# Kernel tuning notes

Hardware: AMD Instinct MI355X
Metric: run time of the kernel (lower is better)

The kernel has to match this reference:

```python
import jax, jax.numpy as jnp
import numpy as np

# dims: T frames, node counts per type, edge counts per relation
T, NA, ND, NB = 48, 1024, 1024, 128
IN, H, HT, OUT = 16, 128, 256, 128
E_AA, E_AD, E_DD, E_AB, E_DB = 8192, 8192, 8192, 2048, 2048


def setup_inputs() -> dict:
    key = jax.random.key(0)
    ks = iter(jax.random.split(key, 48))

    def nrm(shape, scale=0.05):
        return jax.random.normal(next(ks), shape, jnp.float32) * scale

    def edges(e, ns, nd):
        src = jax.random.randint(next(ks), (e,), 0, ns)
        dst = jax.random.randint(next(ks), (e,), 0, nd)
        return jnp.stack([src, dst]).astype(jnp.int32)

    return dict(
        x_attk=jax.random.normal(next(ks), (T, NA, IN), jnp.float32),
        x_def=jax.random.normal(next(ks), (T, ND, IN), jnp.float32),
        x_ball=jax.random.normal(next(ks), (T, NB, IN), jnp.float32),
        ei_aa=edges(E_AA, NA, NA),
        ei_ad=edges(E_AD, NA, ND),
        ei_dd=edges(E_DD, ND, ND),
        ei_ab=edges(E_AB, NA, NB),
        ei_db=edges(E_DB, ND, NB),
        Wp_a=nrm((IN, H)), bp_a=nrm((H,)),
        Wp_d=nrm((IN, H)), bp_d=nrm((H,)),
        Wp_b=nrm((IN, H)), bp_b=nrm((H,)),
        Wg_aa=nrm((H, H)), bg_aa=nrm((H,)),
        Wg_dd=nrm((H, H)), bg_dd=nrm((H,)),
        Wl_ad=nrm((H, H)), Wr_ad=nrm((H, H)), bl_ad=nrm((H,)),
        Wl_ab=nrm((H, H)), Wr_ab=nrm((H, H)), bl_ab=nrm((H,)),
        Wl_db=nrm((H, H)), Wr_db=nrm((H, H)), bl_db=nrm((H,)),
        Wi=nrm((H, 3 * HT)), Wh=nrm((HT, 3 * HT)),
        bi=nrm((3 * HT,)), bh=nrm((3 * HT,)),
        Wout=nrm((3 * HT, OUT)), bout=nrm((OUT,)),
    )


def gcn(x, ei, W, b, n):
    # PyG GCNConv, add_self_loops=False: x' = D^-1/2 A D^-1/2 (x W) + b
    row, col = ei[0], ei[1]
    deg = jnp.zeros((n,), x.dtype).at[col].add(1.0)
    dis = jnp.where(deg > 0, 1.0 / jnp.sqrt(jnp.maximum(deg, 1.0)), 0.0)
    norm = dis[row] * dis[col]                      # [E]
    xw = x @ W                                       # [T, n, H]
    msg = xw[:, row] * norm[None, :, None]           # [T, E, H]
    return jnp.zeros_like(xw).at[:, col].add(msg) + b


def sage(x_src, x_dst, ei, Wl, bl, Wr, nd):
    # PyG SAGEConv (mean aggr): out = mean_j x_j Wl + bl + x_i Wr
    row, col = ei[0], ei[1]
    cnt = jnp.zeros((nd,), x_src.dtype).at[col].add(1.0)
    s = jnp.zeros((x_src.shape[0], nd, x_src.shape[-1]), x_src.dtype)
    s = s.at[:, col].add(x_src[:, row])
    mean = s / jnp.maximum(cnt, 1.0)[None, :, None]
    return mean @ Wl + bl + x_dst @ Wr


def gru_last(z_seq, Wi, Wh, bi, bh):
    # torch GRU (1 layer) final hidden state; z_seq: [T, N, H]
    ht = Wh.shape[0]

    def step(h, x):
        gi = x @ Wi + bi
        gh = h @ Wh + bh
        ir, iz, inn = jnp.split(gi, 3, axis=-1)
        hr, hz, hn = jnp.split(gh, 3, axis=-1)
        r = jax.nn.sigmoid(ir + hr)
        z = jax.nn.sigmoid(iz + hz)
        ncand = jnp.tanh(inn + r * hn)
        return (1.0 - z) * ncand + z * h, None

    h0 = jnp.zeros((z_seq.shape[1], ht), z_seq.dtype)
    hT, _ = jax.lax.scan(step, h0, z_seq)
    return hT                                        # [N, HT]


def _forward(x_attk, x_def, x_ball, ei_aa, ei_ad, ei_dd, ei_ab, ei_db,
             Wp_a, bp_a, Wp_d, bp_d, Wp_b, bp_b,
             Wg_aa, bg_aa, Wg_dd, bg_dd,
             Wl_ad, Wr_ad, bl_ad, Wl_ab, Wr_ab, bl_ab, Wl_db, Wr_db, bl_db,
             Wi, Wh, bi, bh, Wout, bout):
    # per-type node projection (all frames at once)
    pa = x_attk @ Wp_a + bp_a                        # [T, NA, H]
    pd = x_def @ Wp_d + bp_d
    pb = x_ball @ Wp_b + bp_b
    # HeteroConv with sum aggregation across relations per dst type
    z_a = gcn(pa, ei_aa, Wg_aa, bg_aa, NA)
    z_d = gcn(pd, ei_dd, Wg_dd, bg_dd, ND) + sage(pa, pd, ei_ad, Wl_ad, bl_ad, Wr_ad, ND)
    z_b = sage(pa, pb, ei_ab, Wl_ab, bl_ab, Wr_ab, NB) + sage(pd, pb, ei_db, Wl_db, bl_db, Wr_db, NB)
    # temporal GRU over frames, pool final hidden over nodes
    pooled = [gru_last(z, Wi, Wh, bi, bh).mean(axis=0) for z in (z_a, z_d, z_b)]
    return jnp.concatenate(pooled, axis=-1) @ Wout + bout   # [OUT]


def reference(x_attk, x_def, x_ball, ei_aa, ei_ad, ei_dd, ei_ab, ei_db,
              Wp_a, bp_a, Wp_d, bp_d, Wp_b, bp_b,
              Wg_aa, bg_aa, Wg_dd, bg_dd,
              Wl_ad, Wr_ad, bl_ad, Wl_ab, Wr_ab, bl_ab, Wl_db, Wr_db, bl_db,
              Wi, Wh, bi, bh, Wout, bout):
    return _forward(x_attk, x_def, x_ball, ei_aa, ei_ad, ei_dd, ei_ab, ei_db,
                    Wp_a, bp_a, Wp_d, bp_d, Wp_b, bp_b,
                    Wg_aa, bg_aa, Wg_dd, bg_dd,
                    Wl_ad, Wr_ad, bl_ad, Wl_ab, Wr_ab, bl_ab, Wl_db, Wr_db, bl_db,
                    Wi, Wh, bi, bh, Wout, bout)
```

## Files before the change

kernel.cpp:

```cpp
#include <hip/hip_runtime.h>
#include <math.h>

#define TT   48
#define NAA  1024
#define NDD  1024
#define NBB  128
#define NTT  2176
#define INF  16
#define HH   128
#define HTT  256
#define GG   768
#define OUTF 128
#define EAA  8192
#define EAD  8192
#define EDD  8192
#define EAB  2048
#define EDB  2048
#define NEDGE (EAA + EDD + EAD + EAB + EDB)
#define NGRP 136
#define TCH  8

typedef short bf16x8 __attribute__((ext_vector_type(8)));
typedef float f32x4  __attribute__((ext_vector_type(4)));

static const size_t SZ_PB   = (size_t)TT * NTT * HH;
static const size_t OFF_PB  = 0;
static const size_t OFF_ZB  = OFF_PB + SZ_PB / 2;
static const size_t OFF_H0  = OFF_ZB + SZ_PB / 2;
static const size_t OFF_BA  = OFF_H0 + (size_t)NTT * HTT / 2;
static const size_t OFF_BB  = OFF_BA + GG;
static const size_t OFF_WTG = OFF_BB + GG;
static const size_t OFF_BT  = OFF_WTG + 57344;
static const size_t OFF_WIP = OFF_BT + 384;
static const size_t OFF_WHP = OFF_WIP + 49152;
static const size_t OFF_POOL= OFF_WHP + 98304;
static const size_t OFF_PART= OFF_POOL + 1024;
static const size_t OFF_STATS = OFF_PART + 34816;
static const size_t SZ_GI1  = (size_t)TCH * NGRP * 48 * 256 / 2;
static const size_t OFF_GI0 = OFF_STATS + 58400;
static const size_t OFF_GI1 = OFF_GI0 + SZ_GI1;

enum {
  S_CNT_AA=0, S_CNT_DD=1024, S_CNT_AD=2048, S_CNT_AB=3072, S_CNT_DB=3200,
  S_CUR_AA=3328, S_CUR_DD=4352, S_CUR_AD=5376, S_CUR_AB=6400, S_CUR_DB=6528,
  S_ZERO_END=6656,
  S_OFF_AA=6656, S_OFF_DD=7684, S_OFF_AD=8712, S_OFF_AB=9740, S_OFF_DB=9872,
  S_SRC_AA=10004, S_SRC_DD=18196, S_SRC_AD=26388, S_SRC_AB=34580, S_SRC_DB=36628,
  S_NRM_AA=38676, S_NRM_DD=46868,
  S_DIS_AA=55060, S_DIS_DD=56084, S_INV_AD=57108, S_INV_AB=58132, S_INV_DB=58260,
  S_END=58388
};

__device__ __forceinline__ unsigned short f2b(float x) {
  union { float f; unsigned int u; } v; v.f = x;
  unsigned int r = v.u + 0x7FFFu + ((v.u >> 16) & 1u);
  return (unsigned short)(r >> 16);
}
__device__ __forceinline__ float b2f(unsigned short b) {
  union { unsigned int u; float f; } v; v.u = ((unsigned int)b) << 16;
  return v.f;
}

__global__ void count_all(const int* __restrict__ aa, const int* __restrict__ dd,
                          const int* __restrict__ ad, const int* __restrict__ ab,
                          const int* __restrict__ db, int* __restrict__ st) {
  int e = blockIdx.x * 256 + threadIdx.x;
  if (e < EAA) atomicAdd(&st[S_CNT_AA + aa[EAA + e]], 1);
  else if (e < EAA + EDD) atomicAdd(&st[S_CNT_DD + dd[EDD + (e - EAA)]], 1);
  else if (e < EAA + EDD + EAD) atomicAdd(&st[S_CNT_AD + ad[EAD + (e - EAA - EDD)]], 1);
  else if (e < EAA + EDD + EAD + EAB) atomicAdd(&st[S_CNT_AB + ab[EAB + (e - EAA - EDD - EAD)]], 1);
  else if (e < NEDGE) atomicAdd(&st[S_CNT_DB + db[EDB + (e - EAA - EDD - EAD - EAB)]], 1);
}

__global__ __launch_bounds__(1024) void scan5(int* __restrict__ st) {
  __shared__ int buf[1024];
  int b = blockIdx.x, i = threadIdx.x;
  int n, coff, ooff, uoff, soff, isGcn;
  switch (b) {
    case 0:  n = 1024; coff = S_CNT_AA; ooff = S_OFF_AA; uoff = S_CUR_AA; soff = S_DIS_AA; isGcn = 1; break;
    case 1:  n = 1024; coff = S_CNT_DD; ooff = S_OFF_DD; uoff = S_CUR_DD; soff = S_DIS_DD; isGcn = 1; break;
    case 2:  n = 1024; coff = S_CNT_AD; ooff = S_OFF_AD; uoff = S_CUR_AD; soff = S_INV_AD; isGcn = 0; break;
    case 3:  n = 128;  coff = S_CNT_AB; ooff = S_OFF_AB; uoff = S_CUR_AB; soff = S_INV_AB; isGcn = 0; break;
    default: n = 128;  coff = S_CNT_DB; ooff = S_OFF_DB; uoff = S_CUR_DB; soff = S_INV_DB; isGcn = 0; break;
  }
  float* stf = (float*)st;
  int c = (i < n) ? st[coff + i] : 0;
  buf[i] = c;
  __syncthreads();
  for (int s = 1; s < 1024; s <<= 1) {
    int tv = (i >= s) ? buf[i - s] : 0;
    __syncthreads();
    buf[i] += tv;
    __syncthreads();
  }
  if (i < n) {
    int excl = buf[i] - c;
    st[ooff + i] = excl;
    st[uoff + i] = excl;
    if (i == n - 1) st[ooff + n] = buf[i];
    if (isGcn) stf[soff + i] = (c > 0) ? (1.0f / sqrtf((float)c)) : 0.0f;
    else       stf[soff + i] = 1.0f / (float)(c > 0 ? c : 1);
  }
}

__global__ void fill_all(const int* __restrict__ aa, const int* __restrict__ dd,
                         const int* __restrict__ ad, const int* __restrict__ ab,
                         const int* __restrict__ db, int* __restrict__ st) {
  float* stf = (float*)st;
  int e = blockIdx.x * 256 + threadIdx.x;
  if (e < EAA) {
    int s = aa[e], d = aa[EAA + e];
    int pos = atomicAdd(&st[S_CUR_AA + d], 1);
    st[S_SRC_AA + pos] = s;
    stf[S_NRM_AA + pos] = stf[S_DIS_AA + s] * stf[S_DIS_AA + d];
  } else if (e < EAA + EDD) {
    int i = e - EAA;
    int s = dd[i], d = dd[EDD + i];
    int pos = atomicAdd(&st[S_CUR_DD + d], 1);
    st[S_SRC_DD + pos] = s;
    stf[S_NRM_DD + pos] = stf[S_DIS_DD + s] * stf[S_DIS_DD + d];
  } else if (e < EAA + EDD + EAD) {
    int i = e - EAA - EDD;
    int s = ad[i], d = ad[EAD + i];
    int pos = atomicAdd(&st[S_CUR_AD + d], 1);
    st[S_SRC_AD + pos] = s;
  } else if (e < EAA + EDD + EAD + EAB) {
    int i = e - EAA - EDD - EAD;
    int s = ab[i], d = ab[EAB + i];
    int pos = atomicAdd(&st[S_CUR_AB + d], 1);
    st[S_SRC_AB + pos] = s;
  } else if (e < NEDGE) {
    int i = e - EAA - EDD - EAD - EAB;
    int s = db[i], d = db[EDB + i];
    int pos = atomicAdd(&st[S_CUR_DB + d], 1);
    st[S_SRC_DB + pos] = s;
  }
}

__global__ __launch_bounds__(256) void proj64(
    const float* __restrict__ xa, const float* __restrict__ xd, const float* __restrict__ xb,
    const float* __restrict__ Wpa, const float* __restrict__ bpa,
    const float* __restrict__ Wpd, const float* __restrict__ bpd,
    const float* __restrict__ Wpb, const float* __restrict__ bpb,
    unsigned short* __restrict__ Pb) {
  int b = blockIdx.x;
  int t = b / 34, rb = b % 34;
  const float *x, *W, *bias;
  int xrow0;
  if (rb < 16)      { x = xa; W = Wpa; bias = bpa; xrow0 = t * 1024 + rb * 64; }
  else if (rb < 32) { x = xd; W = Wpd; bias = bpd; xrow0 = t * 1024 + (rb - 16) * 64; }
  else              { x = xb; W = Wpb; bias = bpb; xrow0 = t * 128  + (rb - 32) * 64; }
  __shared__ float WS[16][132];
  __shared__ float XS[64][17];
  int tid = threadIdx.x;
  for (int i = tid; i < 2048; i += 256) WS[i >> 7][i & 127] = W[i];
  for (int i = tid; i < 1024; i += 256) XS[i >> 4][i & 15] = x[(size_t)xrow0 * 16 + i];
  __syncthreads();
  int c = tid & 127, rh = tid >> 7;
  float bs = bias[c];
  int row0 = rb * 64;
#pragma unroll 4
  for (int rr = 0; rr < 32; ++rr) {
    int r = rr * 2 + rh;
    float acc = bs;
#pragma unroll
    for (int k = 0; k < 16; ++k) acc = fmaf(XS[r][k], WS[k][c], acc);
    Pb[((size_t)t * NTT + row0 + r) * 128 + c] = f2b(acc);
  }
}

__global__ __launch_bounds__(512) void prep_w(
    const float* __restrict__ Wg_aa, const float* __restrict__ Wg_dd,
    const float* __restrict__ Wl_ad, const float* __restrict__ Wr_ad,
    const float* __restrict__ Wl_ab, const float* __restrict__ Wl_db,
    const float* __restrict__ Wr_ab, const float* __restrict__ Wr_db,
    const float* __restrict__ bg_aa, const float* __restrict__ bg_dd,
    const float* __restrict__ bl_ad, const float* __restrict__ bl_ab,
    const float* __restrict__ bl_db,
    const float* __restrict__ Wi, const float* __restrict__ Wh,
    const float* __restrict__ bi, const float* __restrict__ bh,
    unsigned short* __restrict__ WTgP, float* __restrict__ BT,
    unsigned short* __restrict__ WiP, unsigned short* __restrict__ WhP,
    float* __restrict__ BA, float* __restrict__ BB) {
  int b = blockIdx.x, tid = threadIdx.x;
  if (b < 7) {
    const float* Ws[7] = {Wg_aa, Wg_dd, Wl_ad, Wr_ad, Wl_ab, Wl_db, Wr_ab};
    const float* W1 = Ws[b];
    for (int idx = tid; idx < 16384; idx += 512) {
      int f = idx >> 9, L8 = idx & 511;
      int lane = L8 >> 3, j = L8 & 7;
      int n = (f >> 2) * 16 + (lane & 15);
      int k = (f & 3) * 32 + ((lane >> 4) << 3) + j;
      float v = W1[k * 128 + n];
      if (b == 6) v += Wr_db[k * 128 + n];
      WTgP[(size_t)b * 16384 + idx] = f2b(v);
    }
    if (b == 0 && tid < 128) {
      BT[tid]       = bg_aa[tid];
      BT[128 + tid] = bg_dd[tid] + bl_ad[tid];
      BT[256 + tid] = bl_ab[tid] + bl_db[tid];
    }
  } else if (b < 31) {
    int gid = (b - 7) * 512 + tid;
    int f = gid >> 6, L = gid & 63;
    int w = f / 24, rem = f % 24, ct = rem >> 2, kt = rem & 3;
    int p = w * 96 + ct * 16 + (L & 15);
    int triple = p / 48, g = (p % 48) / 16, cc = p % 16;
    int orig = g * 256 + triple * 16 + cc;
    int k0 = kt * 32 + ((L >> 4) << 3);
    unsigned short out[8];
#pragma unroll
    for (int j = 0; j < 8; ++j) out[j] = f2b(Wi[(size_t)(k0 + j) * GG + orig]);
    *(uint4*)(WiP + (size_t)f * 512 + L * 8) = *(const uint4*)out;
  } else if (b < 415) {
    int f = b - 31;
    int tg = f >> 3, kt = f & 7;
    int lane = tid >> 3, j = tid & 7;
    int triple = tg / 3, g = tg % 3, cc = lane & 15;
    int orig = g * 256 + triple * 16 + cc;
    int k = kt * 32 + ((lane >> 4) << 3) + j;
    WhP[(size_t)f * 512 + tid] = f2b(Wh[(size_t)k * GG + orig]);
  } else {
    for (int p = tid; p < 768; p += 512) {
      int triple = p / 48, g = (p % 48) / 16, cc = p % 16;
      int orig = g * 256 + triple * 16 + cc;
      BA[p] = (g < 2) ? (bi[orig] + bh[orig]) : bi[orig];
      BB[p] = bh[orig];
    }
  }
}

__device__ __forceinline__ void gather_agg(
    const unsigned short* __restrict__ Psrc,
    const int* __restrict__ offs, const int* __restrict__ ssrc,
    const float* __restrict__ snorm, const float* __restrict__ inv,
    int dbase, unsigned short AGG[64][136], int tid) {
  int d_local = tid >> 3;
  int cg = (tid & 7) << 4;
  int d = dbase + d_local;
  int e0 = offs[d], e1 = offs[d + 1];
  float a[16];
#pragma unroll
  for (int j = 0; j < 16; ++j) a[j] = 0.f;
  const unsigned short* pb = Psrc + cg;
  for (int eb = e0; eb < e1; eb += 4) {
    bf16x8 v[4][2];
    float sc[4];
#pragma unroll
    for (int j = 0; j < 4; ++j) {
      int e = eb + j;
      int ec = (e < e1) ? e : (e1 - 1);
      int s = ssrc[ec];
      float scj = snorm ? snorm[ec] : 1.0f;
      if (e >= e1) scj = 0.f;
      sc[j] = scj;
      const unsigned short* pr = pb + (size_t)s * 128;
      v[j][0] = *(const bf16x8*)(pr);
      v[j][1] = *(const bf16x8*)(pr + 8);
    }
#pragma unroll
    for (int j = 0; j < 4; ++j)
#pragma unroll
      for (int c = 0; c < 2; ++c)
#pragma unroll
        for (int i = 0; i < 8; ++i)
          a[c * 8 + i] = fmaf(b2f((unsigned short)v[j][c][i]), sc[j], a[c * 8 + i]);
  }
  float scale = inv ? inv[d] : 1.0f;
#pragma unroll
  for (int j = 0; j < 8; ++j) {
    unsigned int pk = (unsigned int)f2b(a[2 * j] * scale)
                    | ((unsigned int)f2b(a[2 * j + 1] * scale) << 16);
    *(unsigned int*)&AGG[d_local][cg + 2 * j] = pk;
  }
}

__device__ __forceinline__ void mfma_agg(
    const unsigned short AGG[64][136], const unsigned short* __restrict__ wtp,
    f32x4 acc[4], int wr, int fh, int l15, int lk, int lane) {
#pragma unroll
  for (int ks = 0; ks < 4; ++ks) {
    int k = ks * 32 + lk;
    bf16x8 af = *(const bf16x8*)&AGG[wr + l15][k];
#pragma unroll
    for (int fi = 0; fi < 4; ++fi) {
      bf16x8 bfr = *(const bf16x8*)(wtp + (size_t)(((fh + fi) << 2) + ks) * 512 + lane * 8);
      acc[fi] = __builtin_amdgcn_mfma_f32_16x16x32_bf16(af, bfr, acc[fi], 0, 0, 0);
    }
  }
}

__device__ __forceinline__ void mfma_direct(
    const unsigned short* __restrict__ prow, const unsigned short* __restrict__ wtp,
    f32x4 acc[4], int fh, int l15, int lk, int lane) {
#pragma unroll
  for (int ks = 0; ks < 4; ++ks) {
    int k = ks * 32 + lk;
    bf16x8 af = *(const bf16x8*)(prow + k);
#pragma unroll
    for (int fi = 0; fi < 4; ++fi) {
      bf16x8 bfr = *(const bf16x8*)(wtp + (size_t)(((fh + fi) << 2) + ks) * 512 + lane * 8);
      acc[fi] = __builtin_amdgcn_mfma_f32_16x16x32_bf16(af, bfr, acc[fi], 0, 0, 0);
    }
  }
}

__global__ __launch_bounds__(512) void gnn_fused(
    const unsigned short* __restrict__ Pb, unsigned short* __restrict__ Zb,
    const unsigned short* __restrict__ WTgP, const float* __restrict__ BT,
    const int* __restrict__ st) {
  const float* stf = (const float*)st;
  int L = blockIdx.x;
  int slot = L >> 3;
  int t = (L & 7) + ((slot / 34) << 3);
  int rb = slot % 34;
  int row0 = rb * 64;
  int tid = threadIdx.x;
  int w = tid >> 6, lane = tid & 63, l15 = lane & 15, lk = (lane >> 4) * 8;
  int wr = (w >> 1) << 4;
  int fh = (w & 1) << 2;

  __shared__ unsigned short AGG[64][136];

  int typ = (rb < 16) ? 0 : (rb < 32 ? 1 : 2);
  const float* bias = BT + typ * 128;
  f32x4 acc[4];
#pragma unroll
  for (int fi = 0; fi < 4; ++fi) {
    float b = bias[(fh + fi) * 16 + l15];
    f32x4 bv = {b, b, b, b};
    acc[fi] = bv;
  }

  const unsigned short* Pt = Pb + (size_t)t * NTT * 128;
  const unsigned short* prowD = Pt + (size_t)(row0 + wr + l15) * 128;

  if (typ == 0) {
    gather_agg(Pt, st + S_OFF_AA, st + S_SRC_AA, stf + S_NRM_AA, nullptr, row0, AGG, tid);
    __syncthreads();
    mfma_agg(AGG, WTgP + 0 * 16384, acc, wr, fh, l15, lk, lane);
  } else if (typ == 1) {
    int dbase = row0 - 1024;
    gather_agg(Pt + 1024 * 128, st + S_OFF_DD, st + S_SRC_DD, stf + S_NRM_DD, nullptr, dbase, AGG, tid);
    __syncthreads();
    mfma_agg(AGG, WTgP + 1 * 16384, acc, wr, fh, l15, lk, lane);
    __syncthreads();
    gather_agg(Pt, st + S_OFF_AD, st + S_SRC_AD, nullptr, stf + S_INV_AD, dbase, AGG, tid);
    __syncthreads();
    mfma_agg(AGG, WTgP + 2 * 16384, acc, wr, fh, l15, lk, lane);
    mfma_direct(prowD, WTgP + 3 * 16384, acc, fh, l15, lk, lane);
  } else {
    int dbase = row0 - 2048;
    gather_agg(Pt, st + S_OFF_AB, st + S_SRC_AB, nullptr, stf + S_INV_AB, dbase, AGG, tid);
    __syncthreads();
    mfma_agg(AGG, WTgP + 4 * 16384, acc, wr, fh, l15, lk, lane);
    __syncthreads();
    gather_agg(Pt + 1024 * 128, st + S_OFF_DB, st + S_SRC_DB, nullptr, stf + S_INV_DB, dbase, AGG, tid);
    __syncthreads();
    mfma_agg(AGG, WTgP + 5 * 16384, acc, wr, fh, l15, lk, lane);
    mfma_direct(prowD, WTgP + 6 * 16384, acc, fh, l15, lk, lane);
  }

  __syncthreads();
#pragma unroll
  for (int fi = 0; fi < 4; ++fi) {
#pragma unroll
    for (int q = 0; q < 4; ++q) {
      int rl = wr + (lane >> 4) * 4 + q;
      AGG[rl][(fh + fi) * 16 + l15] = f2b(acc[fi][q]);
    }
  }
  __syncthreads();
  unsigned short* ztp = Zb + ((size_t)t * NGRP + (row0 >> 4)) * 4 * 512;
  for (int idx = tid; idx < 1024; idx += 512) {
    int r = idx >> 4, c = (idx & 15) << 3;
    int g = r >> 4;
    int kt = c >> 5;
    int lanePos = ((c >> 3) & 3) * 16 + (r & 15);
    *(uint4*)(ztp + ((size_t)g * 4 + kt) * 512 + lanePos * 8) = *(const uint4*)&AGG[r][c];
  }
}

__global__ __launch_bounds__(256, 2) void gi_gemm(
    const unsigned short* __restrict__ Zb,
    const unsigned short* __restrict__ WiP,
    const float* __restrict__ BA,
    unsigned short* __restrict__ GI, int tbase) {
  int bid = blockIdx.x;
  int tloc = bid / 68, pair = bid % 68;
  int t = tbase + tloc;
  int tid = threadIdx.x, w = tid >> 6, lane = tid & 63, l15 = lane & 15;

  bf16x8 a[2][4];
#pragma unroll
  for (int gl = 0; gl < 2; ++gl) {
    const unsigned short* zf = Zb + (((size_t)t * NGRP + pair * 2 + gl) * 4) * 512 + lane * 8;
#pragma unroll
    for (int kt = 0; kt < 4; ++kt) a[gl][kt] = *(const bf16x8*)(zf + kt * 512);
  }

  f32x4 acc[2][4][3];
#pragma unroll
  for (int trl = 0; trl < 4; ++trl)
#pragma unroll
    for (int g = 0; g < 3; ++g) {
      int triple = w * 4 + trl;
      float b = BA[triple * 48 + g * 16 + l15];
      f32x4 bv = {b, b, b, b};
      acc[0][trl][g] = bv;
      acc[1][trl][g] = bv;
    }

#pragma unroll
  for (int trl = 0; trl < 4; ++trl) {
    int triple = w * 4 + trl;
    int wW = triple >> 1, ctb = (triple & 1) * 3;
#pragma unroll
    for (int g = 0; g < 3; ++g) {
      const unsigned short* wf = WiP + ((size_t)((wW * 6 + ctb + g) * 4)) * 512 + lane * 8;
#pragma unroll
      for (int kt = 0; kt < 4; ++kt) {
        bf16x8 b = *(const bf16x8*)(wf + kt * 512);
        acc[0][trl][g] = __builtin_amdgcn_mfma_f32_16x16x32_bf16(a[0][kt], b, acc[0][trl][g], 0, 0, 0);
        acc[1][trl][g] = __builtin_amdgcn_mfma_f32_16x16x32_bf16(a[1][kt], b, acc[1][trl][g], 0, 0, 0);
      }
    }
  }

#pragma unroll
  for (int gl = 0; gl < 2; ++gl) {
    unsigned short* gout = GI + (((size_t)tloc * NGRP + pair * 2 + gl) * 48) * 256;
#pragma unroll
    for (int trl = 0; trl < 4; ++trl)
#pragma unroll
      for (int g = 0; g < 3; ++g) {
        int triple = w * 4 + trl;
        unsigned short us[4];
#pragma unroll
        for (int q = 0; q < 4; ++q) us[q] = f2b(acc[gl][trl][g][q]);
        *(uint2*)(gout + (size_t)(triple * 3 + g) * 256 + lane * 4) = *(const uint2*)us;
      }
  }
}

#define REC_STEP(GR, GZ, GN, RD, WB, TINV)                                            \
  do {                                                                                \
    f32x4 accR = {0.f, 0.f, 0.f, 0.f};                                                \
    f32x4 accZ = {0.f, 0.f, 0.f, 0.f};                                                \
    f32x4 accNh = {0.f, 0.f, 0.f, 0.f};                                               \
    _Pragma("unroll")                                                                 \
    for (int kt = 0; kt < 8; ++kt) {                                                  \
      bf16x8 a = *(const bf16x8*)&HS2[RD][l15][kt * 32 + lk];                         \
      _Pragma("unroll")                                                               \
      for (int g = 0; g < 3; ++g) {                                                   \
        bf16x8 b;                                                                     \
        if (kt < 6) b = wreg[g][kt];                                                  \
        else b = *(const bf16x8*)&WL[((w * 3 + g) * 2 + (kt - 6)) * 512 +             \
                                     lane * 8 + (TINV)];                              \
        if (g == 0)                                                                   \
          accR = __builtin_amdgcn_mfma_f32_16x16x32_bf16(a, b, accR, 0, 0, 0);        \
        else if (g == 1)                                                              \
          accZ = __builtin_amdgcn_mfma_f32_16x16x32_bf16(a, b, accZ, 0, 0, 0);        \
        else                                                                          \
          accNh = __builtin_amdgcn_mfma_f32_16x16x32_bf16(a, b, accNh, 0, 0, 0);      \
      }                                                                               \
    }                                                                                 \
    unsigned short grs[4], gzs[4], gns[4];                                            \
    *(uint2*)grs = GR; *(uint2*)gzs = GZ; *(uint2*)gns = GN;                          \
    _Pragma("unroll")                                                                 \
    for (int q = 0; q < 4; ++q) {                                                     \
      float rr = 1.f / (1.f + __expf(-(accR[q] + b2f(grs[q]))));                      \
      float zz = 1.f / (1.f + __expf(-(accZ[q] + b2f(gzs[q]))));                      \
      float x2 = 2.f * (b2f(gns[q]) + rr * (accNh[q] + bbn));                         \
      float nn = 1.f - 2.f / (__expf(x2) + 1.f);                                      \
      float hn = (1.f - zz) * nn + zz * hold[q];                                      \
      unsigned short hb = f2b(hn);                                                    \
      hold[q] = b2f(hb);                                                              \
      HS2[WB][qrow + q][w * 16 + l15] = hb;                                           \
    }                                                                                 \
    __syncthreads();                                                                  \
  } while (0)

__global__ __launch_bounds__(1024, 4) void gru_combo(
    const unsigned short* __restrict__ GIcur, unsigned short* __restrict__ GInext,
    const unsigned short* __restrict__ Zb, const unsigned short* __restrict__ WiP,
    const unsigned short* __restrict__ WhP,
    const float* __restrict__ BA, const float* __restrict__ BB,
    unsigned short* __restrict__ Hst, int isFirst, int tbaseNext) {
  __shared__ unsigned short WL[96 * 512];
  __shared__ unsigned short HS2[2][16][262];

  const int tid = threadIdx.x;
  const int w = tid >> 6;
  const int lane = tid & 63;
  const int l15 = lane & 15;
  const int lk = (lane >> 4) << 3;

  if (blockIdx.x >= NGRP) {
    int bid2 = blockIdx.x - NGRP;
    int pair = bid2 % 68, th = bid2 / 68;
#pragma unroll 1
    for (int tl = 0; tl < 4; ++tl) {
      int tloc = th * 4 + tl;
      int t = tbaseNext + tloc;
      bf16x8 a[2][4];
#pragma unroll
      for (int gl = 0; gl < 2; ++gl) {
        const unsigned short* zf = Zb + (((size_t)t * NGRP + pair * 2 + gl) * 4) * 512 + lane * 8;
#pragma unroll
        for (int kt = 0; kt < 4; ++kt) a[gl][kt] = *(const bf16x8*)(zf + kt * 512);
      }
      f32x4 acc[2][3];
#pragma unroll
      for (int g = 0; g < 3; ++g) {
        float b = BA[w * 48 + g * 16 + l15];
        f32x4 bv = {b, b, b, b};
        acc[0][g] = bv;
        acc[1][g] = bv;
      }
      int wW = w >> 1, ctb = (w & 1) * 3;
#pragma unroll
      for (int g = 0; g < 3; ++g) {
        const unsigned short* wf = WiP + ((size_t)((wW * 6 + ctb + g) * 4)) * 512 + lane * 8;
#pragma unroll
        for (int kt = 0; kt < 4; ++kt) {
          bf16x8 b = *(const bf16x8*)(wf + kt * 512);
          acc[0][g] = __builtin_amdgcn_mfma_f32_16x16x32_bf16(a[0][kt], b, acc[0][g], 0, 0, 0);
          acc[1][g] = __builtin_amdgcn_mfma_f32_16x16x32_bf16(a[1][kt], b, acc[1][g], 0, 0, 0);
        }
      }
#pragma unroll
      for (int gl = 0; gl < 2; ++gl) {
        unsigned short* gout = GInext + (((size_t)tloc * NGRP + pair * 2 + gl) * 48) * 256;
#pragma unroll
        for (int g = 0; g < 3; ++g) {
          unsigned short us[4];
#pragma unroll
          for (int q = 0; q < 4; ++q) us[q] = f2b(acc[gl][g][q]);
          *(uint2*)(gout + (size_t)(w * 3 + g) * 256 + lane * 4) = *(const uint2*)us;
        }
      }
    }
    return;
  }

  const int qrow = (lane >> 4) << 2;
  const int node0 = blockIdx.x * 16;

  const unsigned short* gblk = GIcur + ((size_t)blockIdx.x * 48 + w * 3) * 256 + lane * 4;
  const size_t tstep = (size_t)NGRP * 48 * 256;
  uint2 gAr = *(const uint2*)(gblk);
  uint2 gAz = *(const uint2*)(gblk + 256);
  uint2 gAn = *(const uint2*)(gblk + 512);
  uint2 gBr, gBz, gBn;

  for (int idx = tid; idx < 96 * 512; idx += 1024) {
    int fr = idx >> 9, e = idx & 511;
    int tg = fr >> 1, kt2 = fr & 1;
    WL[idx] = WhP[(size_t)(tg * 8 + 6 + kt2) * 512 + e];
  }
  if (isFirst) {
    for (int idx = tid; idx < 16 * 262; idx += 1024) ((unsigned short*)HS2[0])[idx] = 0;
  } else {
    for (int idx = tid; idx < 16 * 256; idx += 1024) {
      int r = idx >> 8, c = idx & 255;
      HS2[0][r][c] = Hst[(size_t)(node0 + r) * 256 + c];
    }
  }

  bf16x8 wreg[3][6];
#pragma unroll
  for (int g = 0; g < 3; ++g)
#pragma unroll
    for (int kt = 0; kt < 6; ++kt)
      wreg[g][kt] = *(const bf16x8*)(WhP + (size_t)((w * 3 + g) * 8 + kt) * 512 + lane * 8);

  const float bbn = BB[w * 48 + 32 + l15];

  float hold[4];
  if (isFirst) {
#pragma unroll
    for (int q = 0; q < 4; ++q) hold[q] = 0.f;
  } else {
#pragma unroll
    for (int q = 0; q < 4; ++q)
      hold[q] = b2f(Hst[(size_t)(node0 + qrow + q) * 256 + w * 16 + l15]);
  }

  __syncthreads();

#pragma unroll 1
  for (int tt = 0; tt < TCH / 2; ++tt) {
    int tinvv = 0;
    asm volatile("" : "+s"(tinvv));

    {
      const unsigned short* gb = gblk + (size_t)(2 * tt + 1) * tstep;
      gBr = *(const uint2*)gb; gBz = *(const uint2*)(gb + 256); gBn = *(const uint2*)(gb + 512);
    }
    REC_STEP(gAr, gAz, gAn, 0, 1, tinvv);
    {
      int tn = (2 * tt + 2 < TCH) ? 2 * tt + 2 : TCH - 1;
      const unsigned short* gb = gblk + (size_t)tn * tstep;
      gAr = *(const uint2*)gb; gAz = *(const uint2*)(gb + 256); gAn = *(const uint2*)(gb + 512);
    }
    REC_STEP(gBr, gBz, gBn, 1, 0, tinvv);
  }

#pragma unroll
  for (int q = 0; q < 4; ++q)
    Hst[(size_t)(node0 + qrow + q) * 256 + w * 16 + l15] = f2b(hold[q]);
}

__global__ __launch_bounds__(256) void pool_part(const unsigned short* __restrict__ Hb,
                                                 float* __restrict__ part) {
  int blk = blockIdx.x;
  int j = threadIdx.x;
  int base = blk * 16;
  float s = 0.f;
  for (int r = 0; r < 16; ++r) s += b2f(Hb[(size_t)(base + r) * 256 + j]);
  part[blk * 256 + j] = s;
}

__global__ __launch_bounds__(256) void pool_final(const float* __restrict__ part,
                                                  float* __restrict__ pooled) {
  int typ = blockIdx.x;
  int j = threadIdx.x;
  int b0 = (typ == 0) ? 0 : (typ == 1 ? 64 : 128);
  int b1 = (typ == 2) ? 136 : b0 + 64;
  float s = 0.f;
  for (int b = b0; b < b1; ++b) s += part[b * 256 + j];
  pooled[typ * 256 + j] = s / (float)((typ == 2) ? 128 : 1024);
}

__global__ __launch_bounds__(128) void out_kernel(
    const float* __restrict__ pooled, const float* __restrict__ Wout,
    const float* __restrict__ bout, float* __restrict__ out) {
  int o = threadIdx.x;
  float acc = bout[o];
  for (int g = 0; g < GG; ++g) acc = fmaf(pooled[g], Wout[g * 128 + o], acc);
  out[o] = acc;
}

extern "C" void kernel_launch(void* const* d_in, const int* in_sizes, int n_in,
                              void* d_out, int out_size, void* d_ws, size_t ws_size,
                              hipStream_t stream) {
  const float* xa    = (const float*)d_in[0];
  const float* xd    = (const float*)d_in[1];
  const float* xb    = (const float*)d_in[2];
  const int*   ei_aa = (const int*)d_in[3];
  const int*   ei_ad = (const int*)d_in[4];
  const int*   ei_dd = (const int*)d_in[5];
  const int*   ei_ab = (const int*)d_in[6];
  const int*   ei_db = (const int*)d_in[7];
  const float* Wp_a = (const float*)d_in[8];  const float* bp_a = (const float*)d_in[9];
  const float* Wp_d = (const float*)d_in[10]; const float* bp_d = (const float*)d_in[11];
  const float* Wp_b = (const float*)d_in[12]; const float* bp_b = (const float*)d_in[13];
  const float* Wg_aa = (const float*)d_in[14]; const float* bg_aa = (const float*)d_in[15];
  const float* Wg_dd = (const float*)d_in[16]; const float* bg_dd = (const float*)d_in[17];
  const float* Wl_ad = (const float*)d_in[18]; const float* Wr_ad = (const float*)d_in[19];
  const float* bl_ad = (const float*)d_in[20];
  const float* Wl_ab = (const float*)d_in[21]; const float* Wr_ab = (const float*)d_in[22];
  const float* bl_ab = (const float*)d_in[23];
  const float* Wl_db = (const float*)d_in[24]; const float* Wr_db = (const float*)d_in[25];
  const float* bl_db = (const float*)d_in[26];
  const float* Wi   = (const float*)d_in[27]; const float* Wh   = (const float*)d_in[28];
  const float* bi   = (const float*)d_in[29]; const float* bh   = (const float*)d_in[30];
  const float* Wout = (const float*)d_in[31]; const float* bout = (const float*)d_in[32];

  float* ws   = (float*)d_ws;
  unsigned short* Pb  = (unsigned short*)(ws + OFF_PB);
  unsigned short* Zb  = (unsigned short*)(ws + OFF_ZB);
  unsigned short* Hst = (unsigned short*)(ws + OFF_H0);
  float* BA = ws + OFF_BA;
  float* BB = ws + OFF_BB;
  unsigned short* WTgP = (unsigned short*)(ws + OFF_WTG);
  float* BT = ws + OFF_BT;
  unsigned short* WiP = (unsigned short*)(ws + OFF_WIP);
  unsigned short* WhP = (unsigned short*)(ws + OFF_WHP);
  float* pooled = ws + OFF_POOL;
  float* part   = ws + OFF_PART;
  int*   st  = (int*)(ws + OFF_STATS);
  unsigned short* GI0 = (unsigned short*)(ws + OFF_GI0);
  unsigned short* GI1 = (unsigned short*)(ws + OFF_GI1);

  hipMemsetAsync(st, 0, (size_t)S_ZERO_END * 4, stream);

  count_all<<<NEDGE / 256, 256, 0, stream>>>(ei_aa, ei_dd, ei_ad, ei_ab, ei_db, st);
  scan5<<<5, 1024, 0, stream>>>(st);
  fill_all<<<NEDGE / 256, 256, 0, stream>>>(ei_aa, ei_dd, ei_ad, ei_ab, ei_db, st);

  proj64<<<TT * 34, 256, 0, stream>>>(xa, xd, xb, Wp_a, bp_a, Wp_d, bp_d, Wp_b, bp_b, Pb);
  prep_w<<<416, 512, 0, stream>>>(Wg_aa, Wg_dd, Wl_ad, Wr_ad, Wl_ab, Wl_db, Wr_ab, Wr_db,
                                  bg_aa, bg_dd, bl_ad, bl_ab, bl_db,
                                  Wi, Wh, bi, bh, WTgP, BT, WiP, WhP, BA, BB);

  gnn_fused<<<TT * 34, 512, 0, stream>>>(Pb, Zb, WTgP, BT, st);

  gi_gemm<<<TCH * 68, 256, 0, stream>>>(Zb, WiP, BA, GI0, 0);
  for (int c = 0; c < 6; ++c) {
    unsigned short* gcur = (c & 1) ? GI1 : GI0;
    unsigned short* gnxt = (c & 1) ? GI0 : GI1;
    int grid = NGRP + ((c < 5) ? 136 : 0);
    gru_combo<<<grid, 1024, 0, stream>>>(gcur, gnxt, Zb, WiP, WhP, BA, BB,
                                         Hst, c == 0, (c + 1) * TCH);
  }

  pool_part<<<NGRP, 256, 0, stream>>>(Hst, part);
  pool_final<<<3, 256, 0, stream>>>(part, pooled);
  out_kernel<<<1, 128, 0, stream>>>(pooled, Wout, bout, (float*)d_out);
}
```

Baseline: 350.8 us.

## Halve GRU block size so each wave computes two hidden-column tiles

The recurrent GRU kernel now launches 512 threads instead of 1024, and each wave handles two 16-column hidden tiles (six gate accumulators) instead of one. Each A fragment read from shared memory is reused across twice as many MFMAs, and the per-step __syncthreads spans fewer waves. The trade-off is a doubled register-resident weight array (wreg 6x6), which raises register pressure and can reduce occupancy or cause spills. The GI-precompute path loops twice per wave to cover the same work.

Measured after the change: 375.3 us. 1.07x slower.

```diff
diff --git a/kernel.cpp b/kernel.cpp
--- a/kernel.cpp
+++ b/kernel.cpp
@@ -443,45 +443,44 @@
   }
 }
 
-#define REC_STEP(GR, GZ, GN, RD, WB, TINV)                                            \
+#define REC_STEP2(GA, RD, WB, TINV)                                                   \
   do {                                                                                \
-    f32x4 accR = {0.f, 0.f, 0.f, 0.f};                                                \
-    f32x4 accZ = {0.f, 0.f, 0.f, 0.f};                                                \
-    f32x4 accNh = {0.f, 0.f, 0.f, 0.f};                                               \
+    f32x4 acc6[6];                                                                    \
+    _Pragma("unroll")                                                                 \
+    for (int g6 = 0; g6 < 6; ++g6) { f32x4 z4 = {0.f,0.f,0.f,0.f}; acc6[g6] = z4; }   \
     _Pragma("unroll")                                                                 \
     for (int kt = 0; kt < 8; ++kt) {                                                  \
       bf16x8 a = *(const bf16x8*)&HS2[RD][l15][kt * 32 + lk];                         \
       _Pragma("unroll")                                                               \
-      for (int g = 0; g < 3; ++g) {                                                   \
+      for (int g6 = 0; g6 < 6; ++g6) {                                                \
         bf16x8 b;                                                                     \
-        if (kt < 6) b = wreg[g][kt];                                                  \
-        else b = *(const bf16x8*)&WL[((w * 3 + g) * 2 + (kt - 6)) * 512 +             \
+        if (kt < 6) b = wreg[g6][kt];                                                 \
+        else b = *(const bf16x8*)&WL[((w2 * 6 + g6) * 2 + (kt - 6)) * 512 +           \
                                      lane * 8 + (TINV)];                              \
-        if (g == 0)                                                                   \
-          accR = __builtin_amdgcn_mfma_f32_16x16x32_bf16(a, b, accR, 0, 0, 0);        \
-        else if (g == 1)                                                              \
-          accZ = __builtin_amdgcn_mfma_f32_16x16x32_bf16(a, b, accZ, 0, 0, 0);        \
-        else                                                                          \
-          accNh = __builtin_amdgcn_mfma_f32_16x16x32_bf16(a, b, accNh, 0, 0, 0);      \
+        acc6[g6] = __builtin_amdgcn_mfma_f32_16x16x32_bf16(a, b, acc6[g6], 0, 0, 0);  \
       }                                                                               \
     }                                                                                 \
-    unsigned short grs[4], gzs[4], gns[4];                                            \
-    *(uint2*)grs = GR; *(uint2*)gzs = GZ; *(uint2*)gns = GN;                          \
     _Pragma("unroll")                                                                 \
-    for (int q = 0; q < 4; ++q) {                                                     \
-      float rr = 1.f / (1.f + __expf(-(accR[q] + b2f(grs[q]))));                      \
-      float zz = 1.f / (1.f + __expf(-(accZ[q] + b2f(gzs[q]))));                      \
-      float x2 = 2.f * (b2f(gns[q]) + rr * (accNh[q] + bbn));                         \
-      float nn = 1.f - 2.f / (__expf(x2) + 1.f);                                      \
-      float hn = (1.f - zz) * nn + zz * hold[q];                                      \
-      unsigned short hb = f2b(hn);                                                    \
-      hold[q] = b2f(hb);                                                              \
-      HS2[WB][qrow + q][w * 16 + l15] = hb;                                           \
+    for (int tr = 0; tr < 2; ++tr) {                                                  \
+      unsigned short grs[4], gzs[4], gns[4];                                          \
+      *(uint2*)grs = GA[tr][0]; *(uint2*)gzs = GA[tr][1]; *(uint2*)gns = GA[tr][2];   \
+      int hcol = (w2 * 2 + tr) * 16 + l15;                                            \
+      _Pragma("unroll")                                                               \
+      for (int q = 0; q < 4; ++q) {                                                   \
+        float rr = 1.f / (1.f + __expf(-(acc6[tr*3+0][q] + b2f(grs[q]))));            \
+        float zz = 1.f / (1.f + __expf(-(acc6[tr*3+1][q] + b2f(gzs[q]))));            \
+        float x2 = 2.f * (b2f(gns[q]) + rr * (acc6[tr*3+2][q] + bbn[tr]));            \
+        float nn = 1.f - 2.f / (__expf(x2) + 1.f);                                    \
+        float hn = (1.f - zz) * nn + zz * hold[tr][q];                                \
+        unsigned short hb = f2b(hn);                                                  \
+        hold[tr][q] = b2f(hb);                                                        \
+        HS2[WB][qrow + q][hcol] = hb;                                                 \
+      }                                                                               \
     }                                                                                 \
     __syncthreads();                                                                  \
   } while (0)
 
-__global__ __launch_bounds__(1024, 4) void gru_combo(
+__global__ __launch_bounds__(512, 2) void gru_combo(
     const unsigned short* __restrict__ GIcur, unsigned short* __restrict__ GInext,
     const unsigned short* __restrict__ Zb, const unsigned short* __restrict__ WiP,
     const unsigned short* __restrict__ WhP,
@@ -491,7 +490,6 @@
   __shared__ unsigned short HS2[2][16][262];
 
   const int tid = threadIdx.x;
-  const int w = tid >> 6;
   const int lane = tid & 63;
   const int l15 = lane & 15;
   const int lk = (lane >> 4) << 3;
@@ -510,81 +508,95 @@
 #pragma unroll
         for (int kt = 0; kt < 4; ++kt) a[gl][kt] = *(const bf16x8*)(zf + kt * 512);
       }
-      f32x4 acc[2][3];
-#pragma unroll
-      for (int g = 0; g < 3; ++g) {
-        float b = BA[w * 48 + g * 16 + l15];
-        f32x4 bv = {b, b, b, b};
-        acc[0][g] = bv;
-        acc[1][g] = bv;
-      }
-      int wW = w >> 1, ctb = (w & 1) * 3;
-#pragma unroll
-      for (int g = 0; g < 3; ++g) {
-        const unsigned short* wf = WiP + ((size_t)((wW * 6 + ctb + g) * 4)) * 512 + lane * 8;
-#pragma unroll
-        for (int kt = 0; kt < 4; ++kt) {
-          bf16x8 b = *(const bf16x8*)(wf + kt * 512);
-          acc[0][g] = __builtin_amdgcn_mfma_f32_16x16x32_bf16(a[0][kt], b, acc[0][g], 0, 0, 0);
-          acc[1][g] = __builtin_amdgcn_mfma_f32_16x16x32_bf16(a[1][kt], b, acc[1][g], 0, 0, 0);
+#pragma unroll 1
+      for (int hw = 0; hw < 2; ++hw) {
+        int w = (tid >> 6) + hw * 8;
+        f32x4 acc[2][3];
+#pragma unroll
+        for (int g = 0; g < 3; ++g) {
+          float b = BA[w * 48 + g * 16 + l15];
+          f32x4 bv = {b, b, b, b};
+          acc[0][g] = bv;
+          acc[1][g] = bv;
+        }
+        int wW = w >> 1, ctb = (w & 1) * 3;
+#pragma unroll
+        for (int g = 0; g < 3; ++g) {
+          const unsigned short* wf = WiP + ((size_t)((wW * 6 + ctb + g) * 4)) * 512 + lane * 8;
+#pragma unroll
+          for (int kt = 0; kt < 4; ++kt) {
+            bf16x8 b = *(const bf16x8*)(wf + kt * 512);
+            acc[0][g] = __builtin_amdgcn_mfma_f32_16x16x32_bf16(a[0][kt], b, acc[0][g], 0, 0, 0);
+            acc[1][g] = __builtin_amdgcn_mfma_f32_16x16x32_bf16(a[1][kt], b, acc[1][g], 0, 0, 0);
+          }
+        }
+#pragma unroll
+        for (int gl = 0; gl < 2; ++gl) {
+          unsigned short* gout = GInext + (((size_t)tloc * NGRP + pair * 2 + gl) * 48) * 256;
+#pragma unroll
+          for (int g = 0; g < 3; ++g) {
+            unsigned short us[4];
+#pragma unroll
+            for (int q = 0; q < 4; ++q) us[q] = f2b(acc[gl][g][q]);
+            *(uint2*)(gout + (size_t)(w * 3 + g) * 256 + lane * 4) = *(const uint2*)us;
+          }
         }
       }
-#pragma unroll
-      for (int gl = 0; gl < 2; ++gl) {
-        unsigned short* gout = GInext + (((size_t)tloc * NGRP + pair * 2 + gl) * 48) * 256;
-#pragma unroll
-        for (int g = 0; g < 3; ++g) {
-          unsigned short us[4];
-#pragma unroll
-          for (int q = 0; q < 4; ++q) us[q] = f2b(acc[gl][g][q]);
-          *(uint2*)(gout + (size_t)(w * 3 + g) * 256 + lane * 4) = *(const uint2*)us;
-        }
-      }
     }
     return;
   }
 
+  const int w2 = tid >> 6;
   const int qrow = (lane >> 4) << 2;
   const int node0 = blockIdx.x * 16;
 
-  const unsigned short* gblk = GIcur + ((size_t)blockIdx.x * 48 + w * 3) * 256 + lane * 4;
+  const unsigned short* gblk0 = GIcur + ((size_t)blockIdx.x * 48 + (w2 * 2 + 0) * 3) * 256 + lane * 4;
+  const unsigned short* gblk1 = GIcur + ((size_t)blockIdx.x * 48 + (w2 * 2 + 1) * 3) * 256 + lane * 4;
   const size_t tstep = (size_t)NGRP * 48 * 256;
-  uint2 gAr = *(const uint2*)(gblk);
-  uint2 gAz = *(const uint2*)(gblk + 256);
-  uint2 gAn = *(const uint2*)(gblk + 512);
-  uint2 gBr, gBz, gBn;
-
-  for (int idx = tid; idx < 96 * 512; idx += 1024) {
+  uint2 gA[2][3], gB[2][3];
+#pragma unroll
+  for (int g = 0; g < 3; ++g) {
+    gA[0][g] = *(const uint2*)(gblk0 + g * 256);
+    gA[1][g] = *(const uint2*)(gblk1 + g * 256);
+  }
+
+  for (int idx = tid; idx < 96 * 512; idx += 512) {
     int fr = idx >> 9, e = idx & 511;
     int tg = fr >> 1, kt2 = fr & 1;
     WL[idx] = WhP[(size_t)(tg * 8 + 6 + kt2) * 512 + e];
   }
   if (isFirst) {
-    for (int idx = tid; idx < 16 * 262; idx += 1024) ((unsigned short*)HS2[0])[idx] = 0;
+    for (int idx = tid; idx < 16 * 262; idx += 512) ((unsigned short*)HS2[0])[idx] = 0;
   } else {
-    for (int idx = tid; idx < 16 * 256; idx += 1024) {
+    for (int idx = tid; idx < 16 * 256; idx += 512) {
       int r = idx >> 8, c = idx & 255;
       HS2[0][r][c] = Hst[(size_t)(node0 + r) * 256 + c];
     }
   }
 
-  bf16x8 wreg[3][6];
-#pragma unroll
-  for (int g = 0; g < 3; ++g)
+  bf16x8 wreg[6][6];
+#pragma unroll
+  for (int g6 = 0; g6 < 6; ++g6)
 #pragma unroll
     for (int kt = 0; kt < 6; ++kt)
-      wreg[g][kt] = *(const bf16x8*)(WhP + (size_t)((w * 3 + g) * 8 + kt) * 512 + lane * 8);
-
-  const float bbn = BB[w * 48 + 32 + l15];
-
-  float hold[4];
+      wreg[g6][kt] = *(const bf16x8*)(WhP + (size_t)((w2 * 6 + g6) * 8 + kt) * 512 + lane * 8);
+
+  float bbn[2];
+#pragma unroll
+  for (int tr = 0; tr < 2; ++tr) bbn[tr] = BB[(w2 * 2 + tr) * 48 + 32 + l15];
+
+  float hold[2][4];
   if (isFirst) {
 #pragma unroll
-    for (int q = 0; q < 4; ++q) hold[q] = 0.f;
+    for (int tr = 0; tr < 2; ++tr)
+#pragma unroll
+      for (int q = 0; q < 4; ++q) hold[tr][q] = 0.f;
   } else {
 #pragma unroll
-    for (int q = 0; q < 4; ++q)
-      hold[q] = b2f(Hst[(size_t)(node0 + qrow + q) * 256 + w * 16 + l15]);
+    for (int tr = 0; tr < 2; ++tr)
+#pragma unroll
+      for (int q = 0; q < 4; ++q)
+        hold[tr][q] = b2f(Hst[(size_t)(node0 + qrow + q) * 256 + (w2 * 2 + tr) * 16 + l15]);
   }
 
   __syncthreads();
@@ -595,21 +607,33 @@
     asm volatile("" : "+s"(tinvv));
 
     {
-      const unsigned short* gb = gblk + (size_t)(2 * tt + 1) * tstep;
-      gBr = *(const uint2*)gb; gBz = *(const uint2*)(gb + 256); gBn = *(const uint2*)(gb + 512);
-    }
-    REC_STEP(gAr, gAz, gAn, 0, 1, tinvv);
+      const unsigned short* g0 = gblk0 + (size_t)(2 * tt + 1) * tstep;
+      const unsigned short* g1 = gblk1 + (size_t)(2 * tt + 1) * tstep;
+#pragma unroll
+      for (int g = 0; g < 3; ++g) {
+        gB[0][g] = *(const uint2*)(g0 + g * 256);
+        gB[1][g] = *(const uint2*)(g1 + g * 256);
+      }
+    }
+    REC_STEP2(gA, 0, 1, tinvv);
     {
       int tn = (2 * tt + 2 < TCH) ? 2 * tt + 2 : TCH - 1;
-      const unsigned short* gb = gblk + (size_t)tn * tstep;
-      gAr = *(const uint2*)gb; gAz = *(const uint2*)(gb + 256); gAn = *(const uint2*)(gb + 512);
-    }
-    REC_STEP(gBr, gBz, gBn, 1, 0, tinvv);
-  }
-
-#pragma unroll
-  for (int q = 0; q < 4; ++q)
-    Hst[(size_t)(node0 + qrow + q) * 256 + w * 16 + l15] = f2b(hold[q]);
+      const unsigned short* g0 = gblk0 + (size_t)tn * tstep;
+      const unsigned short* g1 = gblk1 + (size_t)tn * tstep;
+#pragma unroll
+      for (int g = 0; g < 3; ++g) {
+        gA[0][g] = *(const uint2*)(g0 + g * 256);
+        gA[1][g] = *(const uint2*)(g1 + g * 256);
+      }
+    }
+    REC_STEP2(gB, 1, 0, tinvv);
+  }
+
+#pragma unroll
+  for (int tr = 0; tr < 2; ++tr)
+#pragma unroll
+    for (int q = 0; q < 4; ++q)
+      Hst[(size_t)(node0 + qrow + q) * 256 + (w2 * 2 + tr) * 16 + l15] = f2b(hold[tr][q]);
 }
 
 __global__ __launch_bounds__(256) void pool_part(const unsigned short* __restrict__ Hb,
@@ -702,8 +726,8 @@
     unsigned short* gcur = (c & 1) ? GI1 : GI0;
     unsigned short* gnxt = (c & 1) ? GI0 : GI1;
     int grid = NGRP + ((c < 5) ? 136 : 0);
-    gru_combo<<<grid, 1024, 0, stream>>>(gcur, gnxt, Zb, WiP, WhP, BA, BB,
-                                         Hst, c == 0, (c + 1) * TCH);
+    gru_combo<<<grid, 512, 0, stream>>>(gcur, gnxt, Zb, WiP, WhP, BA, BB,
+                                        Hst, c == 0, (c + 1) * TCH);
   }
 
   pool_part<<<NGRP, 256, 0, stream>>>(Hst, part);
```
